# Performance work log

Hardware: AMD Instinct MI355X
Metric: run time of the kernel (lower is better)

The kernel has to match this reference:

```python
import jax, jax.numpy as jnp
import numpy as np


def binarize(t):
    # torch.where(t > 0, +1, -1)
    return jnp.where(t > 0, jnp.float32(1.0), jnp.float32(-1.0))


def setup_inputs() -> dict:
    key = jax.random.key(0)
    k1, k2, k3 = jax.random.split(key, 3)
    N, D_IN, D_OUT = 8192, 4096, 4096
    x = jax.random.normal(k1, (N, D_IN), dtype=jnp.float32)
    weight = jax.random.normal(k2, (D_OUT, D_IN), dtype=jnp.float32) * 0.02
    bias = jax.random.normal(k3, (D_OUT,), dtype=jnp.float32) * 0.02
    return {"x": x, "weight": weight, "bias": bias}


def reference(x, weight, bias):
    # Binarize input and weight to +/-1, then standard float linear: y = bx @ bw^T + b
    bx = binarize(x)          # [N, D_in]
    bw = binarize(weight)     # [D_out, D_in]
    return jnp.einsum('ni,oi->no', bx, bw) + bias
```

## Files before the change

### kernel.cpp

```cpp
#include <hip/hip_runtime.h>
#include <stdint.h>

using i32x4  = __attribute__((ext_vector_type(4))) int;
using i32x8  = __attribute__((ext_vector_type(8))) int;
using f32x16 = __attribute__((ext_vector_type(16))) float;

#define M_ROWS 8192
#define N_COLS 4096
#define K_DIM  4096
#define KB_ROW 2048
#define BM 256
#define BN 256
#define SC1 0x7F7F7F7F

#define XDW   ((size_t)M_ROWS * K_DIM / 8)
#define TOTDW (((size_t)(M_ROWS + N_COLS)) * K_DIM / 8)

__device__ __forceinline__ unsigned pack8(float4 a, float4 b) {
  unsigned neg =
      ((a.x > 0.f ? 0u : 1u) << 3)  | ((a.y > 0.f ? 0u : 1u) << 7)  |
      ((a.z > 0.f ? 0u : 1u) << 11) | ((a.w > 0.f ? 0u : 1u) << 15) |
      ((b.x > 0.f ? 0u : 1u) << 19) | ((b.y > 0.f ? 0u : 1u) << 23) |
      ((b.z > 0.f ? 0u : 1u) << 27) | ((b.w > 0.f ? 0u : 1u) << 31);
  return 0x22222222u | neg;
}

__global__ __launch_bounds__(256) void binarize_fp4_fused(
    const float4* __restrict__ x, const float4* __restrict__ w,
    uint4* __restrict__ out) {
  size_t u = (size_t)blockIdx.x * blockDim.x + threadIdx.x;
  size_t stride = (size_t)gridDim.x * blockDim.x;
  for (; u < TOTDW / 4; u += stride) {
    size_t d = u * 4;
    const float4* s;
    size_t j;
    if (d < XDW) { s = x; j = d * 2; }
    else         { s = w; j = (d - XDW) * 2; }
    float4 f0 = s[j], f1 = s[j + 1], f2 = s[j + 2], f3 = s[j + 3];
    float4 f4 = s[j + 4], f5 = s[j + 5], f6 = s[j + 6], f7 = s[j + 7];
    uint4 o;
    o.x = pack8(f0, f1);
    o.y = pack8(f2, f3);
    o.z = pack8(f4, f5);
    o.w = pack8(f6, f7);
    out[u] = o;
  }
}

#define GLOAD(gsrc, ldst)                                                    \
  __builtin_amdgcn_global_load_lds(                                          \
      (const __attribute__((address_space(1))) void*)(gsrc),                 \
      (__attribute__((address_space(3))) void*)(ldst), 16, 0, 0)


#define STG_A(NB, KBo, KH)                                                   \
  GLOAD(aS0 + (KBo) + (KH) * 64, As + (NB) + (KH) * 16384 + dstW);           \
  GLOAD(aS1 + (KBo) + (KH) * 64, As + (NB) + (KH) * 16384 + 8192 + dstW)

#define STG_B(NB, KBo, KH)                                                   \
  GLOAD(bS0 + (KBo) + (KH) * 64, Bs + (NB) + (KH) * 16384 + dstW);           \
  GLOAD(bS1 + (KBo) + (KH) * 64, Bs + (NB) + (KH) * 16384 + 8192 + dstW)

#define VM4BAR                                                               \
  asm volatile("s_waitcnt vmcnt(4)" ::: "memory");                           \
  __builtin_amdgcn_s_barrier();

#define VM0BAR                                                               \
  asm volatile("s_waitcnt vmcnt(0)" ::: "memory");                           \
  __builtin_amdgcn_s_barrier();

#define DO_PHASE(BUFOFF, KHOFF, STAGE_STMT, CLOSE_STMT)                      \
  {                                                                          \
    STAGE_STMT                                                               \
    __builtin_amdgcn_s_setprio(1);                                           \
    _Pragma("unroll")                                                        \
    for (int ks = 0; ks < 2; ++ks) {                                         \
      _Pragma("unroll")                                                      \
      for (int nf = 0; nf < 2; ++nf)                                         \
        *(i32x4*)&bf8[nf] = *(const i32x4*)(Bs + (BUFOFF) + (KHOFF) +        \
                                            bBase + nf * 2048 + kv[ks]);     \
      _Pragma("unroll")                                                      \
      for (int mf = 0; mf < 4; ++mf) {                                       \
        *(i32x4*)&af8[mf & 1] = *(const i32x4*)(As + (BUFOFF) + (KHOFF) +    \
                                                aBase + mf * 2048 + kv[ks]); \
        _Pragma("unroll")                                                    \
        for (int nf = 0; nf < 2; ++nf)                                       \
          acc[mf][nf] = __builtin_amdgcn_mfma_scale_f32_32x32x64_f8f6f4(     \
              af8[mf & 1], bf8[nf], acc[mf][nf], 4, 4, 0, SC1, 0, SC1);      \
      }                                                                      \
    }                                                                        \
    __builtin_amdgcn_s_setprio(0);                                           \
    CLOSE_STMT                                                               \
  }

#define TILE(BUF, NBUF, KBo)                                                 \
  DO_PHASE(BUF, 0,     STG_A(NBUF, KBo, 0); STG_B(NBUF, KBo, 0);, VM4BAR)    \
  DO_PHASE(BUF, 16384, STG_A(NBUF, KBo, 1); STG_B(NBUF, KBo, 1);, VM4BAR)

#define TILE_LAST(BUF)                                                       \
  DO_PHASE(BUF, 0, , VM0BAR)                                                 \
  DO_PHASE(BUF, 16384, , )

__global__ __launch_bounds__(512, 2) void bgemm_fp4_32x32(
    const unsigned char* __restrict__ xa, const unsigned char* __restrict__ wb,
    const float* __restrict__ bias, float* __restrict__ y) {
  __shared__ __align__(16) unsigned char As[65536];
  __shared__ __align__(16) unsigned char Bs[65536];

  const int tid  = threadIdx.x;
  const int lane = tid & 63;
  const int w8   = tid >> 6;
  const int wr   = w8 >> 2;
  const int wc   = w8 & 3;

  const int id = blockIdx.x;
  const int sw = ((id & 7) << 6) | (id >> 3);
  const int by = sw >> 4;
  const int bx = sw & 15;
  const int m0 = by * BM;
  const int n0 = bx * BN;

  const int r0  = tid >> 2;
  const int gsl = (((tid & 3) ^ ((tid >> 3) & 3)) << 4);
  const unsigned char* aS0 = xa + (size_t)(m0 + r0) * KB_ROW + gsl;
  const unsigned char* aS1 = xa + (size_t)(m0 + 128 + r0) * KB_ROW + gsl;
  const unsigned char* bS0 = wb + (size_t)(n0 + r0) * KB_ROW + gsl;
  const unsigned char* bS1 = wb + (size_t)(n0 + 128 + r0) * KB_ROW + gsl;
  const int dstW = w8 * 1024;

  const int l31 = lane & 31;
  const int lh  = lane >> 5;
  const int rx  = (l31 >> 1) & 3;
  int kv[2];
  kv[0] = ((0 * 2 + lh) ^ rx) << 4;
  kv[1] = ((1 * 2 + lh) ^ rx) << 4;
  const int aBase = (wr * 128 + l31) * 64;
  const int bBase = (wc * 64 + l31) * 64;

  f32x16 acc[4][2];
#pragma unroll
  for (int i = 0; i < 4; ++i)
#pragma unroll
    for (int j = 0; j < 2; ++j)
#pragma unroll
      for (int e = 0; e < 16; ++e) acc[i][j][e] = 0.f;

  i32x8 af8[2], bf8[2];
#pragma unroll
  for (int i = 0; i < 2; ++i) {
    af8[i] = (i32x8){0, 0, 0, 0, 0, 0, 0, 0};
    bf8[i] = (i32x8){0, 0, 0, 0, 0, 0, 0, 0};
  }

  STG_A(0, 0, 0);
  STG_B(0, 0, 0);
  STG_A(0, 0, 1);
  STG_B(0, 0, 1);
  asm volatile("s_waitcnt vmcnt(4)" ::: "memory");
  __builtin_amdgcn_s_barrier();

#pragma unroll 1
  for (int tp = 0; tp < 7; ++tp) {
    const int kb1 = tp * 256 + 128;
    const int kb2 = tp * 256 + 256;
    TILE(0, 32768, kb1)
    TILE(32768, 0, kb2)
  }
  TILE(0, 32768, 1920)
  TILE_LAST(32768)

  float bv[2];
#pragma unroll
  for (int nf = 0; nf < 2; ++nf) bv[nf] = bias[n0 + wc * 64 + nf * 32 + l31];
#pragma unroll
  for (int mf = 0; mf < 4; ++mf) {
#pragma unroll
    for (int j = 0; j < 16; ++j) {
      const int fr = (j & 3) + 8 * (j >> 2) + 4 * lh;
      const int gr = m0 + wr * 128 + mf * 32 + fr;
      float* orow = y + (size_t)gr * N_COLS + n0 + wc * 64 + l31;
#pragma unroll
      for (int nf = 0; nf < 2; ++nf)
        orow[nf * 32] = acc[mf][nf][j] + bv[nf];
    }
  }
}

extern "C" void kernel_launch(void* const* d_in, const int* in_sizes, int n_in,
                              void* d_out, int out_size, void* d_ws, size_t ws_size,
                              hipStream_t stream) {
  const float* x    = (const float*)d_in[0];
  const float* wgt  = (const float*)d_in[1];
  const float* bias = (const float*)d_in[2];
  float* y = (float*)d_out;

  unsigned char* xa = (unsigned char*)d_ws;
  unsigned char* wb = xa + (size_t)M_ROWS * KB_ROW;

  binarize_fp4_fused<<<3072, 256, 0, stream>>>(
      (const float4*)x, (const float4*)wgt, (uint4*)xa);

  bgemm_fp4_32x32<<<512, 512, 0, stream>>>(xa, wb, bias, y);
}
```

Measured before the change: 130.6 us.

## Split GEMM tile across 16 waves with new LDS layout, nontemporal binarize loads

The FP4 GEMM now runs 1024 threads (16 waves) per 256x256 block instead of 512. Each wave owns a 64x64 sub-tile with a 2x2 accumulator grid rather than 128x64 with 4x2. The LDS staging is reorganised: half the threads load A and half load B, using a new unswizzled layout with simpler read addressing. The binarize pass also switches to nontemporal loads. More waves can hide latency, but each wave does less MFMA work per LDS fragment load, the LDS layout may cause bank conflicts, and the 128KB of LDS still caps occupancy at one block per CU despite the launch_bounds hint.

```diff
diff --git a/kernel.cpp b/kernel.cpp
--- a/kernel.cpp
+++ b/kernel.cpp
@@ -4,6 +4,7 @@
 using i32x4  = __attribute__((ext_vector_type(4))) int;
 using i32x8  = __attribute__((ext_vector_type(8))) int;
 using f32x16 = __attribute__((ext_vector_type(16))) float;
+using f32x4v = __attribute__((ext_vector_type(4))) float;
 
 #define M_ROWS 8192
 #define N_COLS 4096
@@ -16,28 +17,34 @@
 #define XDW   ((size_t)M_ROWS * K_DIM / 8)
 #define TOTDW (((size_t)(M_ROWS + N_COLS)) * K_DIM / 8)
 
-__device__ __forceinline__ unsigned pack8(float4 a, float4 b) {
+__device__ __forceinline__ unsigned pack8(f32x4v a, f32x4v b) {
   unsigned neg =
-      ((a.x > 0.f ? 0u : 1u) << 3)  | ((a.y > 0.f ? 0u : 1u) << 7)  |
-      ((a.z > 0.f ? 0u : 1u) << 11) | ((a.w > 0.f ? 0u : 1u) << 15) |
-      ((b.x > 0.f ? 0u : 1u) << 19) | ((b.y > 0.f ? 0u : 1u) << 23) |
-      ((b.z > 0.f ? 0u : 1u) << 27) | ((b.w > 0.f ? 0u : 1u) << 31);
+      ((a[0] > 0.f ? 0u : 1u) << 3)  | ((a[1] > 0.f ? 0u : 1u) << 7)  |
+      ((a[2] > 0.f ? 0u : 1u) << 11) | ((a[3] > 0.f ? 0u : 1u) << 15) |
+      ((b[0] > 0.f ? 0u : 1u) << 19) | ((b[1] > 0.f ? 0u : 1u) << 23) |
+      ((b[2] > 0.f ? 0u : 1u) << 27) | ((b[3] > 0.f ? 0u : 1u) << 31);
   return 0x22222222u | neg;
 }
 
 __global__ __launch_bounds__(256) void binarize_fp4_fused(
-    const float4* __restrict__ x, const float4* __restrict__ w,
+    const f32x4v* __restrict__ x, const f32x4v* __restrict__ w,
     uint4* __restrict__ out) {
   size_t u = (size_t)blockIdx.x * blockDim.x + threadIdx.x;
   size_t stride = (size_t)gridDim.x * blockDim.x;
   for (; u < TOTDW / 4; u += stride) {
     size_t d = u * 4;
-    const float4* s;
+    const f32x4v* s;
     size_t j;
     if (d < XDW) { s = x; j = d * 2; }
     else         { s = w; j = (d - XDW) * 2; }
-    float4 f0 = s[j], f1 = s[j + 1], f2 = s[j + 2], f3 = s[j + 3];
-    float4 f4 = s[j + 4], f5 = s[j + 5], f6 = s[j + 6], f7 = s[j + 7];
+    f32x4v f0 = __builtin_nontemporal_load(&s[j]);
+    f32x4v f1 = __builtin_nontemporal_load(&s[j + 1]);
+    f32x4v f2 = __builtin_nontemporal_load(&s[j + 2]);
+    f32x4v f3 = __builtin_nontemporal_load(&s[j + 3]);
+    f32x4v f4 = __builtin_nontemporal_load(&s[j + 4]);
+    f32x4v f5 = __builtin_nontemporal_load(&s[j + 5]);
+    f32x4v f6 = __builtin_nontemporal_load(&s[j + 6]);
+    f32x4v f7 = __builtin_nontemporal_load(&s[j + 7]);
     uint4 o;
     o.x = pack8(f0, f1);
     o.y = pack8(f2, f3);
@@ -53,55 +60,55 @@
       (__attribute__((address_space(3))) void*)(ldst), 16, 0, 0)
 
 
-#define STG_A(NB, KBo, KH)                                                   \
-  GLOAD(aS0 + (KBo) + (KH) * 64, As + (NB) + (KH) * 16384 + dstW);           \
-  GLOAD(aS1 + (KBo) + (KH) * 64, As + (NB) + (KH) * 16384 + 8192 + dstW)
-
-#define STG_B(NB, KBo, KH)                                                   \
-  GLOAD(bS0 + (KBo) + (KH) * 64, Bs + (NB) + (KH) * 16384 + dstW);           \
-  GLOAD(bS1 + (KBo) + (KH) * 64, Bs + (NB) + (KH) * 16384 + 8192 + dstW)
-
-#define VM4BAR                                                               \
-  asm volatile("s_waitcnt vmcnt(4)" ::: "memory");                           \
+#define VM2BAR                                                               \
+  asm volatile("s_waitcnt vmcnt(2)" ::: "memory");                           \
   __builtin_amdgcn_s_barrier();
 
 #define VM0BAR                                                               \
   asm volatile("s_waitcnt vmcnt(0)" ::: "memory");                           \
   __builtin_amdgcn_s_barrier();
 
-#define DO_PHASE(BUFOFF, KHOFF, STAGE_STMT, CLOSE_STMT)                      \
+#define STG(KH, NB, KBo)                                                     \
+  GLOAD(sBase + (KBo) + (KH) * 64, lBase + (NB) + (KH) * 16384);             \
+  GLOAD(sBase + (KBo) + (KH) * 64 + 262144,                                  \
+        lBase + (NB) + (KH) * 16384 + 8192)
+
+#define DO_PHASE(BUF, KH, STAGE_STMT, CLOSE_STMT)                            \
   {                                                                          \
     STAGE_STMT                                                               \
     __builtin_amdgcn_s_setprio(1);                                           \
     _Pragma("unroll")                                                        \
     for (int ks = 0; ks < 2; ++ks) {                                         \
-      _Pragma("unroll")                                                      \
-      for (int nf = 0; nf < 2; ++nf)                                         \
-        *(i32x4*)&bf8[nf] = *(const i32x4*)(Bs + (BUFOFF) + (KHOFF) +        \
-                                            bBase + nf * 2048 + kv[ks]);     \
-      _Pragma("unroll")                                                      \
-      for (int mf = 0; mf < 4; ++mf) {                                       \
-        *(i32x4*)&af8[mf & 1] = *(const i32x4*)(As + (BUFOFF) + (KHOFF) +    \
-                                                aBase + mf * 2048 + kv[ks]); \
-        _Pragma("unroll")                                                    \
-        for (int nf = 0; nf < 2; ++nf)                                       \
-          acc[mf][nf] = __builtin_amdgcn_mfma_scale_f32_32x32x64_f8f6f4(     \
-              af8[mf & 1], bf8[nf], acc[mf][nf], 4, 4, 0, SC1, 0, SC1);      \
-      }                                                                      \
+      *(i32x4*)&bf8[0] =                                                     \
+          *(const i32x4*)(bRd + (BUF) + (KH) + ks * 1024);                   \
+      *(i32x4*)&bf8[1] =                                                     \
+          *(const i32x4*)(bRd + (BUF) + (KH) + 2048 + ks * 1024);            \
+      *(i32x4*)&af8[0] =                                                     \
+          *(const i32x4*)(aRd + (BUF) + (KH) + ks * 1024);                   \
+      *(i32x4*)&af8[1] =                                                     \
+          *(const i32x4*)(aRd + (BUF) + (KH) + 2048 + ks * 1024);            \
+      acc[0][0] = __builtin_amdgcn_mfma_scale_f32_32x32x64_f8f6f4(           \
+          af8[0], bf8[0], acc[0][0], 4, 4, 0, SC1, 0, SC1);                  \
+      acc[0][1] = __builtin_amdgcn_mfma_scale_f32_32x32x64_f8f6f4(           \
+          af8[0], bf8[1], acc[0][1], 4, 4, 0, SC1, 0, SC1);                  \
+      acc[1][0] = __builtin_amdgcn_mfma_scale_f32_32x32x64_f8f6f4(           \
+          af8[1], bf8[0], acc[1][0], 4, 4, 0, SC1, 0, SC1);                  \
+      acc[1][1] = __builtin_amdgcn_mfma_scale_f32_32x32x64_f8f6f4(           \
+          af8[1], bf8[1], acc[1][1], 4, 4, 0, SC1, 0, SC1);                  \
     }                                                                        \
     __builtin_amdgcn_s_setprio(0);                                           \
     CLOSE_STMT                                                               \
   }
 
-#define TILE(BUF, NBUF, KBo)                                                 \
-  DO_PHASE(BUF, 0,     STG_A(NBUF, KBo, 0); STG_B(NBUF, KBo, 0);, VM4BAR)    \
-  DO_PHASE(BUF, 16384, STG_A(NBUF, KBo, 1); STG_B(NBUF, KBo, 1);, VM4BAR)
+#define TILE(BUF, NB, KBo)                                                   \
+  DO_PHASE(BUF, 0,     STG(0, NB, KBo);, VM2BAR)                             \
+  DO_PHASE(BUF, 16384, STG(1, NB, KBo);, VM2BAR)
 
 #define TILE_LAST(BUF)                                                       \
   DO_PHASE(BUF, 0, , VM0BAR)                                                 \
   DO_PHASE(BUF, 16384, , )
 
-__global__ __launch_bounds__(512, 2) void bgemm_fp4_32x32(
+__global__ __launch_bounds__(1024, 4) void bgemm_fp4_16w(
     const unsigned char* __restrict__ xa, const unsigned char* __restrict__ wb,
     const float* __restrict__ bias, float* __restrict__ y) {
   __shared__ __align__(16) unsigned char As[65536];
@@ -109,37 +116,30 @@
 
   const int tid  = threadIdx.x;
   const int lane = tid & 63;
-  const int w8   = tid >> 6;
-  const int wr   = w8 >> 2;
-  const int wc   = w8 & 3;
+  const int w16  = tid >> 6;
+  const int wr   = w16 >> 2;
+  const int wc   = w16 & 3;
 
   const int id = blockIdx.x;
   const int sw = ((id & 7) << 6) | (id >> 3);
-  const int by = sw >> 4;
-  const int bx = sw & 15;
-  const int m0 = by * BM;
-  const int n0 = bx * BN;
-
-  const int r0  = tid >> 2;
-  const int gsl = (((tid & 3) ^ ((tid >> 3) & 3)) << 4);
-  const unsigned char* aS0 = xa + (size_t)(m0 + r0) * KB_ROW + gsl;
-  const unsigned char* aS1 = xa + (size_t)(m0 + 128 + r0) * KB_ROW + gsl;
-  const unsigned char* bS0 = wb + (size_t)(n0 + r0) * KB_ROW + gsl;
-  const unsigned char* bS1 = wb + (size_t)(n0 + 128 + r0) * KB_ROW + gsl;
-  const int dstW = w8 * 1024;
-
-  const int l31 = lane & 31;
-  const int lh  = lane >> 5;
-  const int rx  = (l31 >> 1) & 3;
-  int kv[2];
-  kv[0] = ((0 * 2 + lh) ^ rx) << 4;
-  kv[1] = ((1 * 2 + lh) ^ rx) << 4;
-  const int aBase = (wr * 128 + l31) * 64;
-  const int bBase = (wc * 64 + l31) * 64;
-
-  f32x16 acc[4][2];
-#pragma unroll
-  for (int i = 0; i < 4; ++i)
+  const int m0 = (sw >> 4) * BM;
+  const int n0 = (sw & 15) * BN;
+
+  const int c   = tid & 511;
+  const int rl  = ((c >> 7) << 5) + (c & 31);
+  const int col = ((c >> 5) & 3) << 4;
+  const int isB = tid >> 9;
+  const unsigned char* sBase =
+      isB ? (wb + (size_t)(n0 + rl) * KB_ROW + col)
+          : (xa + (size_t)(m0 + rl) * KB_ROW + col);
+  unsigned char* lBase = (isB ? Bs : As) + ((w16 & 7) << 10);
+
+  const unsigned char* aRd = As + wr * 4096 + lane * 16;
+  const unsigned char* bRd = Bs + wc * 4096 + lane * 16;
+
+  f32x16 acc[2][2];
+#pragma unroll
+  for (int i = 0; i < 2; ++i)
 #pragma unroll
     for (int j = 0; j < 2; ++j)
 #pragma unroll
@@ -152,11 +152,9 @@
     bf8[i] = (i32x8){0, 0, 0, 0, 0, 0, 0, 0};
   }
 
-  STG_A(0, 0, 0);
-  STG_B(0, 0, 0);
-  STG_A(0, 0, 1);
-  STG_B(0, 0, 1);
-  asm volatile("s_waitcnt vmcnt(4)" ::: "memory");
+  STG(0, 0, 0);
+  STG(1, 0, 0);
+  asm volatile("s_waitcnt vmcnt(2)" ::: "memory");
   __builtin_amdgcn_s_barrier();
 
 #pragma unroll 1
@@ -169,19 +167,20 @@
   TILE(0, 32768, 1920)
   TILE_LAST(32768)
 
+  const int l31 = lane & 31;
+  const int lh  = lane >> 5;
   float bv[2];
 #pragma unroll
   for (int nf = 0; nf < 2; ++nf) bv[nf] = bias[n0 + wc * 64 + nf * 32 + l31];
 #pragma unroll
-  for (int mf = 0; mf < 4; ++mf) {
+  for (int mf = 0; mf < 2; ++mf) {
 #pragma unroll
     for (int j = 0; j < 16; ++j) {
       const int fr = (j & 3) + 8 * (j >> 2) + 4 * lh;
-      const int gr = m0 + wr * 128 + mf * 32 + fr;
+      const int gr = m0 + wr * 64 + mf * 32 + fr;
       float* orow = y + (size_t)gr * N_COLS + n0 + wc * 64 + l31;
-#pragma unroll
-      for (int nf = 0; nf < 2; ++nf)
-        orow[nf * 32] = acc[mf][nf][j] + bv[nf];
+      orow[0]  = acc[mf][0][j] + bv[0];
+      orow[32] = acc[mf][1][j] + bv[1];
     }
   }
 }
@@ -198,7 +197,7 @@
   unsigned char* wb = xa + (size_t)M_ROWS * KB_ROW;
 
   binarize_fp4_fused<<<3072, 256, 0, stream>>>(
-      (const float4*)x, (const float4*)wgt, (uint4*)xa);
-
-  bgemm_fp4_32x32<<<512, 512, 0, stream>>>(xa, wb, bias, y);
-}
+      (const f32x4v*)x, (const f32x4v*)wgt, (uint4*)xa);
+
+  bgemm_fp4_16w<<<512, 1024, 0, stream>>>(xa, wb, bias, y);
+}
```

Result: slower. 174.4 us (+33.5%).
